# Kernel tuning notes

Hardware: AMD Instinct MI355X
Metric: run time of the kernel (lower is better)

The kernel has to match this reference:

```python
import jax, jax.numpy as jnp
import numpy as np

N = 50000      # nodes per graph batch (per side)
E = 600000     # edges per side
B = 4096       # number of graphs (drug pairs)
D = 128        # node_dim == hidden_dim
K = 128        # kge_dim
R = 86         # rel_total
L = 3          # n_iter
EPS = 1e-5


def setup_inputs() -> dict:
    key = jax.random.key(0)
    ks = jax.random.split(key, 16)
    inp = {}
    inp["x1"] = jax.random.normal(ks[0], (N, D), jnp.float32)
    inp["x2"] = jax.random.normal(ks[1], (N, D), jnp.float32)
    inp["edge_index1"] = jax.random.randint(ks[2], (2, E), 0, N)
    inp["edge_index2"] = jax.random.randint(ks[3], (2, E), 0, N)
    inp["batch1"] = jnp.sort(jax.random.randint(ks[4], (N,), 0, B))
    inp["batch2"] = jnp.sort(jax.random.randint(ks[5], (N,), 0, B))
    inp["rel"] = jax.random.randint(ks[6], (B,), 0, R)
    # SAGEConv params, stacked over L layers (all [D,D] since node_dim==hidden_dim)
    sc = 0.05
    inp["Wl"] = jax.random.normal(ks[7], (L, D, D), jnp.float32) * sc   # lin on aggregated neighbors (has bias)
    inp["bl"] = jnp.zeros((L, D), jnp.float32)
    inp["Wr"] = jax.random.normal(ks[8], (L, D, D), jnp.float32) * sc   # root (self) lin, no bias
    # BatchNorm (eval mode: running stats)
    inp["bn_gamma"] = jnp.ones((L, D), jnp.float32)
    inp["bn_beta"] = jnp.zeros((L, D), jnp.float32)
    inp["bn_mean"] = jnp.zeros((L, D), jnp.float32)
    inp["bn_var"] = jnp.ones((L, D), jnp.float32)
    # relation embedding + final MLP
    inp["kge"] = jax.random.normal(ks[9], (R, K), jnp.float32)
    inp["W1"] = jax.random.normal(ks[10], (2 * D + K, D), jnp.float32) * sc
    inp["b1"] = jnp.zeros((D,), jnp.float32)
    inp["W2"] = jax.random.normal(ks[11], (D, 1), jnp.float32) * sc
    inp["b2"] = jnp.zeros((1,), jnp.float32)
    return inp


def _gnn(x, edge_index, Wl, bl, Wr, g, b, m, v):
    src, dst = edge_index[0], edge_index[1]
    deg = jax.ops.segment_sum(jnp.ones((E,), x.dtype), dst, num_segments=N)
    deg = jnp.maximum(deg, 1.0)[:, None]
    for i in range(L):
        agg = jax.ops.segment_sum(x[src], dst, num_segments=N) / deg  # mean aggregation
        h = agg @ Wl[i] + bl[i] + x @ Wr[i]                           # SAGEConv
        h = (h - m[i]) * (g[i] / jnp.sqrt(v[i] + EPS)) + b[i]         # BN (eval)
        x = jax.nn.relu(h)                                            # dropout = identity (eval)
    return x


def reference(x1, edge_index1, batch1, x2, edge_index2, batch2, rel,
              Wl, bl, Wr, bn_gamma, bn_beta, bn_mean, bn_var,
              kge, W1, b1, W2, b2):
    h1 = _gnn(x1, edge_index1, Wl, bl, Wr, bn_gamma, bn_beta, bn_mean, bn_var)
    h2 = _gnn(x2, edge_index2, Wl, bl, Wr, bn_gamma, bn_beta, bn_mean, bn_var)
    p1 = jax.ops.segment_sum(h1, batch1, num_segments=B)  # global_add_pool
    p2 = jax.ops.segment_sum(h2, batch2, num_segments=B)
    r = kge[rel]                                          # [B, K]
    z = jnp.concatenate([p1, p2, r], axis=-1)             # [B, 2D+K]
    h = jax.nn.relu(z @ W1 + b1)
    out = h @ W2 + b2
    return out.reshape(-1)
```

## Files before the change

kernel.cpp:

```cpp
#include <hip/hip_runtime.h>

#define NN 50000
#define NE 600000
#define NB 4096
#define DD 128
#define EPSV 1e-5f
#define NBKT 196
#define NCHUNK 256
#define CHSZ ((NE + NCHUNK - 1) / NCHUNK)

typedef __bf16 bf16x8 __attribute__((ext_vector_type(8)));
typedef float f32x4 __attribute__((ext_vector_type(4)));

__device__ inline unsigned short f2bf(float f) {
    unsigned u = __float_as_uint(f);
    u = (u + 0x7FFFu + ((u >> 16) & 1u)) >> 16;
    return (unsigned short)u;
}
__device__ inline float bf2f(unsigned short h) {
    return __uint_as_float(((unsigned)h) << 16);
}

__global__ void k_cvt(const float* __restrict__ x1, const float* __restrict__ x2,
                      unsigned short* __restrict__ xh, unsigned short* __restrict__ xl) {
    int i = blockIdx.x * 256 + threadIdx.x;
    if (i >= 2 * NN * 32) return;
    const float* x = (i < NN * 32) ? x1 : x2;
    int j = (i < NN * 32) ? i : i - NN * 32;
    float4 v = ((const float4*)x)[j];
    ushort4 h, l;
    h.x = f2bf(v.x); l.x = f2bf(v.x - bf2f(h.x));
    h.y = f2bf(v.y); l.y = f2bf(v.y - bf2f(h.y));
    h.z = f2bf(v.z); l.z = f2bf(v.z - bf2f(h.z));
    h.w = f2bf(v.w); l.w = f2bf(v.w - bf2f(h.w));
    ((ushort4*)xh)[i] = h;
    ((ushort4*)xl)[i] = l;
}

__global__ void k_wcvt(const float* __restrict__ Wl, const float* __restrict__ Wr,
                       const float* __restrict__ W1, unsigned* __restrict__ wtp) {
    int t = blockIdx.x * 256 + threadIdx.x;
    if (t >= 3 * 128 * 256 + 128 * 384) return;
    float w;
    int idx;
    if (t < 3 * 128 * 256) {
        int k = t & 255;
        int n = (t >> 8) & 127;
        int l = t >> 15;
        w = (k < 128) ? Wl[l * 16384 + k * 128 + n] : Wr[l * 16384 + (k - 128) * 128 + n];
        idx = t;
    } else {
        int u = t - 3 * 128 * 256;
        int n = u / 384;
        int k = u - n * 384;
        w = W1[k * 128 + n];
        idx = t;
    }
    unsigned short h = f2bf(w);
    unsigned short l = f2bf(w - bf2f(h));
    wtp[idx] = ((unsigned)h << 16) | (unsigned)l;
}

__global__ void k_hist(const int* __restrict__ d0, const int* __restrict__ d1,
                       int* __restrict__ bcnt) {
    int side = (blockIdx.x >= NCHUNK) ? 1 : 0;
    int c = blockIdx.x - side * NCHUNK;
    const int* dst = side ? d1 : d0;
    int tid = threadIdx.x;
    __shared__ int h[NBKT];
    for (int i = tid; i < NBKT; i += 256) h[i] = 0;
    __syncthreads();
    int e0 = c * CHSZ, e1 = min(e0 + CHSZ, NE);
    for (int e = e0 + tid; e < e1; e += 256) atomicAdd(&h[dst[e] >> 8], 1);
    __syncthreads();
    int* bc = bcnt + ((size_t)side * NCHUNK + c) * NBKT;
    for (int i = tid; i < NBKT; i += 256) bc[i] = h[i];
}

__global__ void k_s1(int* __restrict__ bcnt, int* __restrict__ btot) {
    int side = (blockIdx.x >= NBKT) ? 1 : 0;
    int b = blockIdx.x - side * NBKT;
    int tid = threadIdx.x;
    int idx = ((size_t)side * NCHUNK + tid) * NBKT + b;
    int v = bcnt[idx];
    int lane = tid & 63, wv = tid >> 6;
    int x = v;
#pragma unroll
    for (int off = 1; off < 64; off <<= 1) {
        int y = __shfl_up(x, off, 64);
        if (lane >= off) x += y;
    }
    __shared__ int ws4[4];
    if (lane == 63) ws4[wv] = x;
    __syncthreads();
    int add = 0;
#pragma unroll
    for (int w = 0; w < 4; w++)
        if (w < wv) add += ws4[w];
    int incl = x + add;
    bcnt[idx] = incl - v;
    if (tid == 255) btot[side * NBKT + b] = incl;
}

__global__ void k_s2(const int* __restrict__ btot, int* __restrict__ bbase,
                     int* __restrict__ ptrC) {
    int side = blockIdx.x;
    int tid = threadIdx.x;
    int v = (tid < NBKT) ? btot[side * NBKT + tid] : 0;
    int lane = tid & 63, wv = tid >> 6;
    int x = v;
#pragma unroll
    for (int off = 1; off < 64; off <<= 1) {
        int y = __shfl_up(x, off, 64);
        if (lane >= off) x += y;
    }
    __shared__ int ws4[4];
    if (lane == 63) ws4[wv] = x;
    __syncthreads();
    int add = 0;
#pragma unroll
    for (int w = 0; w < 4; w++)
        if (w < wv) add += ws4[w];
    int incl = x + add;
    if (tid < NBKT) bbase[side * NBKT + tid] = incl - v;
    if (tid == 0 && side == 1) ptrC[2 * NN] = 2 * NE;
}

__global__ void k_part(const int* __restrict__ s0, const int* __restrict__ d0,
                       const int* __restrict__ s1, const int* __restrict__ d1,
                       const int* __restrict__ bcnt, const int* __restrict__ bbase,
                       int* __restrict__ part) {
    int side = (blockIdx.x >= NCHUNK) ? 1 : 0;
    int c = blockIdx.x - side * NCHUNK;
    const int* src = side ? s1 : s0;
    const int* dst = side ? d1 : d0;
    int tid = threadIdx.x;
    __shared__ int off[NBKT];
    const int* bc = bcnt + ((size_t)side * NCHUNK + c) * NBKT;
    for (int i = tid; i < NBKT; i += 256) off[i] = bbase[side * NBKT + i] + bc[i];
    __syncthreads();
    int e0 = c * CHSZ, e1 = min(e0 + CHSZ, NE);
    int* P = part + (size_t)side * NE;
    int soff = side * NN;
    for (int e = e0 + tid; e < e1; e += 256) {
        int d = dst[e];
        int pos = atomicAdd(&off[d >> 8], 1);
        P[pos] = ((src[e] + soff) << 8) | (d & 255);
    }
}

__global__ void k_csr(const int* __restrict__ part, const int* __restrict__ bbase,
                      int* __restrict__ ptrC, float* __restrict__ invdC,
                      int* __restrict__ csrC) {
    int side = (blockIdx.x >= NBKT) ? 1 : 0;
    int b = blockIdx.x - side * NBKT;
    int tid = threadIdx.x;
    const int* P = part + (size_t)side * NE;
    int base = bbase[side * NBKT + b];
    int endp = (b == NBKT - 1) ? NE : bbase[side * NBKT + b + 1];
    __shared__ int cnt[256];
    cnt[tid] = 0;
    __syncthreads();
    for (int e = base + tid; e < endp; e += 256) atomicAdd(&cnt[P[e] & 255], 1);
    __syncthreads();
    int v = cnt[tid];
    int lane = tid & 63, wv = tid >> 6;
    int x = v;
#pragma unroll
    for (int off = 1; off < 64; off <<= 1) {
        int y = __shfl_up(x, off, 64);
        if (lane >= off) x += y;
    }
    __shared__ int ws4[4];
    if (lane == 63) ws4[wv] = x;
    __syncthreads();
    int add = 0;
#pragma unroll
    for (int w = 0; w < 4; w++)
        if (w < wv) add += ws4[w];
    int excl = x + add - v;
    int node = (b << 8) + tid;
    if (node < NN) {
        ptrC[side * NN + node] = side * NE + base + excl;
        invdC[side * NN + node] = 1.0f / (float)(v > 1 ? v : 1);
    }
    __syncthreads();
    cnt[tid] = excl;
    __syncthreads();
    for (int e = base + tid; e < endp; e += 256) {
        int p = P[e];
        int pos = atomicAdd(&cnt[p & 255], 1);
        csrC[(size_t)side * NE + base + pos] = p >> 8;
    }
}

__global__ void k_gather(const unsigned short* __restrict__ xh, const int* __restrict__ ptr,
                         const int* __restrict__ csr, const float* __restrict__ invd,
                         unsigned short* __restrict__ aggH) {
    int wid = threadIdx.x >> 6;
    int lane = threadIdx.x & 63;
    int q = lane >> 4;
    int c = lane & 15;
    int n = blockIdx.x * 4 + wid;
    if (n >= 2 * NN) return;
    int beg = ptr[n], end = ptr[n + 1];
    float id = invd[n];
    float a[8];
#pragma unroll
    for (int k = 0; k < 8; k++) a[k] = 0.f;

    for (int base = beg; base < end; base += 64) {
        int cnt = min(end - base, 64);
        int idxv = csr[base + min(lane, cnt - 1)];
        for (int e0 = 0; e0 < cnt; e0 += 8) {
            int eA = e0 + q;
            int eB = e0 + 4 + q;
            int iA = __shfl(idxv, eA, 64);
            int iB = __shfl(idxv, eB, 64);
            float wA = (eA < cnt) ? 1.f : 0.f;
            float wB = (eB < cnt) ? 1.f : 0.f;
            uint4 vA = *(const uint4*)(xh + (((unsigned)iA << 7) + (c << 3)));
            uint4 vB = *(const uint4*)(xh + (((unsigned)iB << 7) + (c << 3)));
            a[0] += wA * __uint_as_float(vA.x << 16);
            a[1] += wA * __uint_as_float(vA.x & 0xffff0000u);
            a[2] += wA * __uint_as_float(vA.y << 16);
            a[3] += wA * __uint_as_float(vA.y & 0xffff0000u);
            a[4] += wA * __uint_as_float(vA.z << 16);
            a[5] += wA * __uint_as_float(vA.z & 0xffff0000u);
            a[6] += wA * __uint_as_float(vA.w << 16);
            a[7] += wA * __uint_as_float(vA.w & 0xffff0000u);
            a[0] += wB * __uint_as_float(vB.x << 16);
            a[1] += wB * __uint_as_float(vB.x & 0xffff0000u);
            a[2] += wB * __uint_as_float(vB.y << 16);
            a[3] += wB * __uint_as_float(vB.y & 0xffff0000u);
            a[4] += wB * __uint_as_float(vB.z << 16);
            a[5] += wB * __uint_as_float(vB.z & 0xffff0000u);
            a[6] += wB * __uint_as_float(vB.w << 16);
            a[7] += wB * __uint_as_float(vB.w & 0xffff0000u);
        }
    }
#pragma unroll
    for (int k = 0; k < 8; k++) {
        a[k] += __shfl_xor(a[k], 16, 64);
        a[k] += __shfl_xor(a[k], 32, 64);
    }
    if (q == 0) {
        unsigned short h0 = f2bf(a[0] * id), h1 = f2bf(a[1] * id);
        unsigned short h2 = f2bf(a[2] * id), h3 = f2bf(a[3] * id);
        unsigned short h4 = f2bf(a[4] * id), h5 = f2bf(a[5] * id);
        unsigned short h6 = f2bf(a[6] * id), h7 = f2bf(a[7] * id);
        uint4 o;
        o.x = (unsigned)h0 | ((unsigned)h1 << 16);
        o.y = (unsigned)h2 | ((unsigned)h3 << 16);
        o.z = (unsigned)h4 | ((unsigned)h5 << 16);
        o.w = (unsigned)h6 | ((unsigned)h7 << 16);
        *(uint4*)(aggH + (size_t)n * DD + c * 8) = o;
    }
}

__launch_bounds__(256)
__global__ void k_gemm(const unsigned short* __restrict__ AH,
                       const unsigned short* __restrict__ XH, const unsigned short* __restrict__ XL,
                       const unsigned* __restrict__ Wtp,
                       const float* __restrict__ bl, const float* __restrict__ g,
                       const float* __restrict__ be, const float* __restrict__ mn,
                       const float* __restrict__ vr,
                       unsigned short* __restrict__ OH, unsigned short* __restrict__ OL,
                       float* __restrict__ Of, int f32out) {
    __shared__ __align__(16) unsigned short sA[2][64 * 40];
    __shared__ __align__(16) unsigned short sW[2][64 * 40];
    int tid = threadIdx.x;
    int gx = blockIdx.x;
    int m0 = (gx >> 1) * 64;
    int n0 = (gx & 1) * 64;
    int lane = tid & 63;
    int w = tid >> 6;
    int fm = lane & 15, q = lane >> 4;
    int wr = (w & 1) * 32;
    int wn = (w >> 1) * 32;

    f32x4 acc[2][2];
#pragma unroll
    for (int i = 0; i < 2; i++)
#pragma unroll
        for (int j = 0; j < 2; j++) acc[i][j] = (f32x4){0.f, 0.f, 0.f, 0.f};

    for (int c = 0; c < 8; c++) {
        int isA = (c < 4);
        const unsigned short* SH = isA ? AH : XH;
        const unsigned short* SL = isA ? (const unsigned short*)0 : XL;
        int k0 = (c & 3) * 32;
        int k0W = c * 32;
        __syncthreads();
#pragma unroll
        for (int i = 0; i < 2; i++) {
            int u = tid + 256 * i;
            int row = u >> 3, seg = u & 7;
            int grow = m0 + row;
            size_t goff = (size_t)grow * DD + k0 + seg * 4;
            ushort4 hv = make_ushort4(0, 0, 0, 0);
            if (grow < 2 * NN) hv = *(const ushort4*)(SH + goff);
            *(ushort4*)&sA[0][row * 40 + seg * 4] = hv;
            if (!isA) {
                ushort4 lv = make_ushort4(0, 0, 0, 0);
                if (grow < 2 * NN) lv = *(const ushort4*)(SL + goff);
                *(ushort4*)&sA[1][row * 40 + seg * 4] = lv;
            }
        }
#pragma unroll
        for (int i = 0; i < 2; i++) {
            int u = tid + 256 * i;
            int row = u >> 3, seg = u & 7;
            uint4 val = *(const uint4*)(Wtp + (size_t)(n0 + row) * 256 + k0W + seg * 4);
            ushort4 hi, lo;
            hi.x = val.x >> 16; hi.y = val.y >> 16; hi.z = val.z >> 16; hi.w = val.w >> 16;
            lo.x = val.x & 0xFFFF; lo.y = val.y & 0xFFFF; lo.z = val.z & 0xFFFF; lo.w = val.w & 0xFFFF;
            *(ushort4*)&sW[0][row * 40 + seg * 4] = hi;
            *(ushort4*)&sW[1][row * 40 + seg * 4] = lo;
        }
        __syncthreads();
        bf16x8 afh[2], afl[2];
#pragma unroll
        for (int mt = 0; mt < 2; mt++) {
            int r = wr + mt * 16 + fm;
            afh[mt] = *(const bf16x8*)&sA[0][r * 40 + q * 8];
            if (!isA) afl[mt] = *(const bf16x8*)&sA[1][r * 40 + q * 8];
        }
#pragma unroll
        for (int nt = 0; nt < 2; nt++) {
            int nr = wn + nt * 16 + fm;
            bf16x8 wh = *(const bf16x8*)&sW[0][nr * 40 + q * 8];
            bf16x8 wl = *(const bf16x8*)&sW[1][nr * 40 + q * 8];
#pragma unroll
            for (int mt = 0; mt < 2; mt++) {
                acc[mt][nt] = __builtin_amdgcn_mfma_f32_16x16x32_bf16(afh[mt], wh, acc[mt][nt], 0, 0, 0);
                acc[mt][nt] = __builtin_amdgcn_mfma_f32_16x16x32_bf16(afh[mt], wl, acc[mt][nt], 0, 0, 0);
                if (!isA)
                    acc[mt][nt] = __builtin_amdgcn_mfma_f32_16x16x32_bf16(afl[mt], wh, acc[mt][nt], 0, 0, 0);
            }
        }
    }

    float scv[2], shv[2];
#pragma unroll
    for (int nt = 0; nt < 2; nt++) {
        int jj = n0 + wn + nt * 16 + fm;
        float s = g[jj] * rsqrtf(vr[jj] + EPSV);
        scv[nt] = s;
        shv[nt] = (bl[jj] - mn[jj]) * s + be[jj];
    }
#pragma unroll
    for (int mt = 0; mt < 2; mt++) {
#pragma unroll
        for (int r = 0; r < 4; r++) {
            int grow = m0 + wr + mt * 16 + q * 4 + r;
            if (grow < 2 * NN) {
#pragma unroll
                for (int nt = 0; nt < 2; nt++) {
                    int gcol = n0 + wn + nt * 16 + fm;
                    float o = fmaxf(acc[mt][nt][r] * scv[nt] + shv[nt], 0.f);
                    if (f32out) {
                        Of[(size_t)grow * DD + gcol] = o;
                    } else {
                        unsigned short h = f2bf(o);
                        OH[(size_t)grow * DD + gcol] = h;
                        OL[(size_t)grow * DD + gcol] = f2bf(o - bf2f(h));
                    }
                }
            }
        }
    }
}

__launch_bounds__(128)
__global__ void k_pool2(const float* __restrict__ cf, const int* __restrict__ bt1,
                        const int* __restrict__ bt2, float* __restrict__ ppool) {
    int side = (blockIdx.x >= NB) ? 1 : 0;
    int b = blockIdx.x - side * NB;
    const int* batch = side ? bt2 : bt1;
    const float* h = cf + (size_t)side * NN * DD;
    __shared__ int sr[2];
    if (threadIdx.x < 2) {
        int target = b + (int)threadIdx.x;
        int lo = 0, hi = NN;
        while (lo < hi) {
            int mid = (lo + hi) >> 1;
            if (batch[mid] < target) lo = mid + 1; else hi = mid;
        }
        sr[threadIdx.x] = lo;
    }
    __syncthreads();
    int beg = sr[0], end = sr[1];
    int t = threadIdx.x;
    float acc = 0.f;
    for (int r = beg; r < end; r++) acc += h[(size_t)r * DD + t];
    ppool[((size_t)side * NB + b) * DD + t] = acc;
}

__global__ void k_zb(const float* __restrict__ ppool, const int* __restrict__ rel,
                     const float* __restrict__ kge,
                     unsigned short* __restrict__ zh, unsigned short* __restrict__ zl) {
    int t = blockIdx.x * 256 + threadIdx.x;
    if (t >= NB * 384) return;
    int b = t / 384;
    int j = t - b * 384;
    float v;
    if (j < 128) v = ppool[(size_t)b * DD + j];
    else if (j < 256) v = ppool[(size_t)NB * DD + (size_t)b * DD + (j - 128)];
    else v = kge[(size_t)rel[b] * 128 + (j - 256)];
    unsigned short h = f2bf(v);
    zh[t] = h;
    zl[t] = f2bf(v - bf2f(h));
}

__launch_bounds__(256)
__global__ void k_mlp2(const unsigned short* __restrict__ zh, const unsigned short* __restrict__ zl,
                       const unsigned* __restrict__ w1p,
                       const float* __restrict__ b1, const float* __restrict__ W2,
                       const float* __restrict__ b2, float* __restrict__ out) {
    __shared__ __align__(16) unsigned short sZ[2][32 * 40];
    __shared__ __align__(16) unsigned short sW[2][128 * 40];
    __shared__ float hpart[32][4];
    int tid = threadIdx.x;
    int m0 = blockIdx.x * 32;
    int lane = tid & 63, w = tid >> 6;
    int fm = lane & 15, q = lane >> 4;
    int wn = w * 32;

    f32x4 acc[2][2];
#pragma unroll
    for (int i = 0; i < 2; i++)
#pragma unroll
        for (int j = 0; j < 2; j++) acc[i][j] = (f32x4){0.f, 0.f, 0.f, 0.f};

    for (int c = 0; c < 12; c++) {
        int k0 = c * 32;
        __syncthreads();
        {
            int row = tid >> 3, seg = tid & 7;
            size_t off = (size_t)(m0 + row) * 384 + k0 + seg * 4;
            *(ushort4*)&sZ[0][row * 40 + seg * 4] = *(const ushort4*)(zh + off);
            *(ushort4*)&sZ[1][row * 40 + seg * 4] = *(const ushort4*)(zl + off);
        }
#pragma unroll
        for (int i = 0; i < 4; i++) {
            int u = tid + 256 * i;
            int row = u >> 3, seg = u & 7;
            uint4 val = *(const uint4*)(w1p + (size_t)row * 384 + k0 + seg * 4);
            ushort4 hi, lo;
            hi.x = val.x >> 16; hi.y = val.y >> 16; hi.z = val.z >> 16; hi.w = val.w >> 16;
            lo.x = val.x & 0xFFFF; lo.y = val.y & 0xFFFF; lo.z = val.z & 0xFFFF; lo.w = val.w & 0xFFFF;
            *(ushort4*)&sW[0][row * 40 + seg * 4] = hi;
            *(ushort4*)&sW[1][row * 40 + seg * 4] = lo;
        }
        __syncthreads();
        bf16x8 zfh[2], zfl[2];
#pragma unroll
        for (int mt = 0; mt < 2; mt++) {
            int r = mt * 16 + fm;
            zfh[mt] = *(const bf16x8*)&sZ[0][r * 40 + q * 8];
            zfl[mt] = *(const bf16x8*)&sZ[1][r * 40 + q * 8];
        }
#pragma unroll
        for (int nt = 0; nt < 2; nt++) {
            int nr = wn + nt * 16 + fm;
            bf16x8 wh = *(const bf16x8*)&sW[0][nr * 40 + q * 8];
            bf16x8 wl = *(const bf16x8*)&sW[1][nr * 40 + q * 8];
#pragma unroll
            for (int mt = 0; mt < 2; mt++) {
                acc[mt][nt] = __builtin_amdgcn_mfma_f32_16x16x32_bf16(zfh[mt], wh, acc[mt][nt], 0, 0, 0);
                acc[mt][nt] = __builtin_amdgcn_mfma_f32_16x16x32_bf16(zfh[mt], wl, acc[mt][nt], 0, 0, 0);
                acc[mt][nt] = __builtin_amdgcn_mfma_f32_16x16x32_bf16(zfl[mt], wh, acc[mt][nt], 0, 0, 0);
            }
        }
    }

    float b1v[2], w2v[2];
#pragma unroll
    for (int nt = 0; nt < 2; nt++) {
        int col = wn + nt * 16 + fm;
        b1v[nt] = b1[col];
        w2v[nt] = W2[col];
    }
#pragma unroll
    for (int mt = 0; mt < 2; mt++) {
#pragma unroll
        for (int r = 0; r < 4; r++) {
            float val = 0.f;
#pragma unroll
            for (int nt = 0; nt < 2; nt++)
                val += fmaxf(acc[mt][nt][r] + b1v[nt], 0.f) * w2v[nt];
#pragma unroll
            for (int m = 1; m < 16; m <<= 1) val += __shfl_xor(val, m, 64);
            if (fm == 0) hpart[mt * 16 + q * 4 + r][w] = val;
        }
    }
    __syncthreads();
    if (tid < 32)
        out[m0 + tid] = hpart[tid][0] + hpart[tid][1] + hpart[tid][2] + hpart[tid][3] + b2[0];
}

extern "C" void kernel_launch(void* const* d_in, const int* in_sizes, int n_in,
                              void* d_out, int out_size, void* d_ws, size_t ws_size,
                              hipStream_t stream) {
    const float* x1  = (const float*)d_in[0];
    const float* x2  = (const float*)d_in[1];
    const int*   ei1 = (const int*)d_in[2];
    const int*   ei2 = (const int*)d_in[3];
    const int*   bt1 = (const int*)d_in[4];
    const int*   bt2 = (const int*)d_in[5];
    const int*   rel = (const int*)d_in[6];
    const float* Wl  = (const float*)d_in[7];
    const float* bl  = (const float*)d_in[8];
    const float* Wr  = (const float*)d_in[9];
    const float* g   = (const float*)d_in[10];
    const float* be  = (const float*)d_in[11];
    const float* mn  = (const float*)d_in[12];
    const float* vr  = (const float*)d_in[13];
    const float* kge = (const float*)d_in[14];
    const float* W1  = (const float*)d_in[15];
    const float* b1v = (const float*)d_in[16];
    const float* W2  = (const float*)d_in[17];
    const float* b2v = (const float*)d_in[18];

    char* ws = (char*)d_ws;
    size_t off = 0;
    auto alloc = [&](size_t bytes) {
        void* p = ws + off;
        off += (bytes + 255) & ~(size_t)255;
        return p;
    };
    const size_t PL = (size_t)2 * NN * DD;
    unsigned short* xbufH = (unsigned short*)alloc(PL * 2);
    unsigned short* xbufL = (unsigned short*)alloc(PL * 2);
    unsigned short* obufH = (unsigned short*)alloc(PL * 2);
    unsigned short* obufL = (unsigned short*)alloc(PL * 2);
    unsigned short* aggH  = (unsigned short*)alloc(PL * 2);
    unsigned* wtp  = (unsigned*)alloc((size_t)(3 * 128 * 256 + 128 * 384) * 4);
    float* ppool   = (float*)alloc((size_t)2 * NB * DD * 4);
    unsigned short* zh = (unsigned short*)alloc((size_t)NB * 384 * 2);
    unsigned short* zl = (unsigned short*)alloc((size_t)NB * 384 * 2);
    int*   bcnt    = (int*)alloc((size_t)2 * NCHUNK * NBKT * 4);
    int*   btot    = (int*)alloc((size_t)2 * NBKT * 4);
    int*   bbase   = (int*)alloc((size_t)2 * NBKT * 4);
    int*   part    = (int*)alloc((size_t)2 * NE * 4);
    int*   ptrC    = (int*)alloc((size_t)(2 * NN + 1) * 4);
    float* invdC   = (float*)alloc((size_t)2 * NN * 4);
    int*   csrC    = (int*)alloc((size_t)2 * NE * 4);
    if (off > ws_size) return;

    float* cf = (float*)obufH;

    const int nbCvt   = 12500;
    const int nbNode4 = (2 * NN + 3) / 4;
    const int nbGemm  = ((2 * NN + 63) / 64) * 2;
    const int nbW     = (3 * 128 * 256 + 128 * 384 + 255) / 256;

    k_wcvt<<<nbW, 256, 0, stream>>>(Wl, Wr, W1, wtp);

    k_hist<<<2 * NCHUNK, 256, 0, stream>>>(ei1 + NE, ei2 + NE, bcnt);
    k_s1<<<2 * NBKT, 256, 0, stream>>>(bcnt, btot);
    k_s2<<<2, 256, 0, stream>>>(btot, bbase, ptrC);
    k_part<<<2 * NCHUNK, 256, 0, stream>>>(ei1, ei1 + NE, ei2, ei2 + NE, bcnt, bbase, part);
    k_csr<<<2 * NBKT, 256, 0, stream>>>(part, bbase, ptrC, invdC, csrC);

    k_cvt<<<nbCvt, 256, 0, stream>>>(x1, x2, xbufH, xbufL);

    k_gather<<<nbNode4, 256, 0, stream>>>(xbufH, ptrC, csrC, invdC, aggH);
    k_gemm<<<nbGemm, 256, 0, stream>>>(aggH, xbufH, xbufL, wtp, bl, g, be, mn, vr,
                                       obufH, obufL, (float*)nullptr, 0);
    k_gather<<<nbNode4, 256, 0, stream>>>(obufH, ptrC, csrC, invdC, aggH);
    k_gemm<<<nbGemm, 256, 0, stream>>>(aggH, obufH, obufL, wtp + 32768, bl + 128, g + 128,
                                       be + 128, mn + 128, vr + 128,
                                       xbufH, xbufL, (float*)nullptr, 0);
    k_gather<<<nbNode4, 256, 0, stream>>>(xbufH, ptrC, csrC, invdC, aggH);
    k_gemm<<<nbGemm, 256, 0, stream>>>(aggH, xbufH, xbufL, wtp + 65536, bl + 256, g + 256,
                                       be + 256, mn + 256, vr + 256,
                                       (unsigned short*)nullptr, (unsigned short*)nullptr, cf, 1);

    k_pool2<<<2 * NB, 128, 0, stream>>>(cf, bt1, bt2, ppool);
    k_zb<<<(NB * 384 + 255) / 256, 256, 0, stream>>>(ppool, rel, kge, zh, zl);
    k_mlp2<<<NB / 32, 256, 0, stream>>>(zh, zl, wtp + 98304, b1v, W2, b2v, (float*)d_out);
}
```

Before: 454.5 us.

## Widen GEMM tile to full 128 columns, pre-split weights, fuse pool with z build

The SAGE GEMM now uses one block per 128 rows covering all 128 output columns (4x4 MFMA tiles per wave). Each activation row is loaded once instead of twice, with 16-byte loads in place of 8-byte ones. Weights are pre-laid out as separate hi/lo bf16 planes per K-chunk, so the GEMM copies them straight into shared memory without unpacking. Pooling is fused with building the concatenated bf16 z input, and the gather accumulates into float2 vectors. The larger tile raises register and LDS use per block and halves the block count, which may reduce occupancy.

```diff
diff --git a/kernel.cpp b/kernel.cpp
--- a/kernel.cpp
+++ b/kernel.cpp
@@ -11,6 +11,7 @@
 
 typedef __bf16 bf16x8 __attribute__((ext_vector_type(8)));
 typedef float f32x4 __attribute__((ext_vector_type(4)));
+typedef float f32x2 __attribute__((ext_vector_type(2)));
 
 __device__ inline unsigned short f2bf(float f) {
     unsigned u = __float_as_uint(f);
@@ -38,27 +39,29 @@
 }
 
 __global__ void k_wcvt(const float* __restrict__ Wl, const float* __restrict__ Wr,
-                       const float* __restrict__ W1, unsigned* __restrict__ wtp) {
+                       const float* __restrict__ W1,
+                       unsigned short* __restrict__ wfp, unsigned* __restrict__ w1p) {
     int t = blockIdx.x * 256 + threadIdx.x;
-    if (t >= 3 * 128 * 256 + 128 * 384) return;
-    float w;
-    int idx;
     if (t < 3 * 128 * 256) {
         int k = t & 255;
         int n = (t >> 8) & 127;
         int l = t >> 15;
-        w = (k < 128) ? Wl[l * 16384 + k * 128 + n] : Wr[l * 16384 + (k - 128) * 128 + n];
-        idx = t;
-    } else {
+        float w = (k < 128) ? Wl[l * 16384 + k * 128 + n] : Wr[l * 16384 + (k - 128) * 128 + n];
+        unsigned short h = f2bf(w);
+        unsigned short lo = f2bf(w - bf2f(h));
+        int c = k >> 5, kk = k & 31;
+        size_t base = (size_t)l * 65536 + (size_t)c * 8192 + n * 32 + kk;
+        wfp[base] = h;
+        wfp[base + 4096] = lo;
+    } else if (t < 3 * 128 * 256 + 128 * 384) {
         int u = t - 3 * 128 * 256;
         int n = u / 384;
         int k = u - n * 384;
-        w = W1[k * 128 + n];
-        idx = t;
-    }
-    unsigned short h = f2bf(w);
-    unsigned short l = f2bf(w - bf2f(h));
-    wtp[idx] = ((unsigned)h << 16) | (unsigned)l;
+        float w = W1[k * 128 + n];
+        unsigned short h = f2bf(w);
+        unsigned short l = f2bf(w - bf2f(h));
+        w1p[u] = ((unsigned)h << 16) | (unsigned)l;
+    }
 }
 
 __global__ void k_hist(const int* __restrict__ d0, const int* __restrict__ d1,
@@ -205,9 +208,9 @@
     if (n >= 2 * NN) return;
     int beg = ptr[n], end = ptr[n + 1];
     float id = invd[n];
-    float a[8];
-#pragma unroll
-    for (int k = 0; k < 8; k++) a[k] = 0.f;
+    f32x2 a2[4];
+#pragma unroll
+    for (int k = 0; k < 4; k++) a2[k] = (f32x2){0.f, 0.f};
 
     for (int base = beg; base < end; base += 64) {
         int cnt = min(end - base, 64);
@@ -217,28 +220,25 @@
             int eB = e0 + 4 + q;
             int iA = __shfl(idxv, eA, 64);
             int iB = __shfl(idxv, eB, 64);
-            float wA = (eA < cnt) ? 1.f : 0.f;
-            float wB = (eB < cnt) ? 1.f : 0.f;
+            f32x2 wA2 = (eA < cnt) ? (f32x2){1.f, 1.f} : (f32x2){0.f, 0.f};
+            f32x2 wB2 = (eB < cnt) ? (f32x2){1.f, 1.f} : (f32x2){0.f, 0.f};
             uint4 vA = *(const uint4*)(xh + (((unsigned)iA << 7) + (c << 3)));
             uint4 vB = *(const uint4*)(xh + (((unsigned)iB << 7) + (c << 3)));
-            a[0] += wA * __uint_as_float(vA.x << 16);
-            a[1] += wA * __uint_as_float(vA.x & 0xffff0000u);
-            a[2] += wA * __uint_as_float(vA.y << 16);
-            a[3] += wA * __uint_as_float(vA.y & 0xffff0000u);
-            a[4] += wA * __uint_as_float(vA.z << 16);
-            a[5] += wA * __uint_as_float(vA.z & 0xffff0000u);
-            a[6] += wA * __uint_as_float(vA.w << 16);
-            a[7] += wA * __uint_as_float(vA.w & 0xffff0000u);
-            a[0] += wB * __uint_as_float(vB.x << 16);
-            a[1] += wB * __uint_as_float(vB.x & 0xffff0000u);
-            a[2] += wB * __uint_as_float(vB.y << 16);
-            a[3] += wB * __uint_as_float(vB.y & 0xffff0000u);
-            a[4] += wB * __uint_as_float(vB.z << 16);
-            a[5] += wB * __uint_as_float(vB.z & 0xffff0000u);
-            a[6] += wB * __uint_as_float(vB.w << 16);
-            a[7] += wB * __uint_as_float(vB.w & 0xffff0000u);
-        }
-    }
+            a2[0] += wA2 * (f32x2){__uint_as_float(vA.x << 16), __uint_as_float(vA.x & 0xffff0000u)};
+            a2[1] += wA2 * (f32x2){__uint_as_float(vA.y << 16), __uint_as_float(vA.y & 0xffff0000u)};
+            a2[2] += wA2 * (f32x2){__uint_as_float(vA.z << 16), __uint_as_float(vA.z & 0xffff0000u)};
+            a2[3] += wA2 * (f32x2){__uint_as_float(vA.w << 16), __uint_as_float(vA.w & 0xffff0000u)};
+            a2[0] += wB2 * (f32x2){__uint_as_float(vB.x << 16), __uint_as_float(vB.x & 0xffff0000u)};
+            a2[1] += wB2 * (f32x2){__uint_as_float(vB.y << 16), __uint_as_float(vB.y & 0xffff0000u)};
+            a2[2] += wB2 * (f32x2){__uint_as_float(vB.z << 16), __uint_as_float(vB.z & 0xffff0000u)};
+            a2[3] += wB2 * (f32x2){__uint_as_float(vB.w << 16), __uint_as_float(vB.w & 0xffff0000u)};
+        }
+    }
+    float a[8];
+    a[0] = a2[0][0]; a[1] = a2[0][1];
+    a[2] = a2[1][0]; a[3] = a2[1][1];
+    a[4] = a2[2][0]; a[5] = a2[2][1];
+    a[6] = a2[3][0]; a[7] = a2[3][1];
 #pragma unroll
     for (int k = 0; k < 8; k++) {
         a[k] += __shfl_xor(a[k], 16, 64);
@@ -259,105 +259,101 @@
 }
 
 __launch_bounds__(256)
-__global__ void k_gemm(const unsigned short* __restrict__ AH,
-                       const unsigned short* __restrict__ XH, const unsigned short* __restrict__ XL,
-                       const unsigned* __restrict__ Wtp,
-                       const float* __restrict__ bl, const float* __restrict__ g,
-                       const float* __restrict__ be, const float* __restrict__ mn,
-                       const float* __restrict__ vr,
-                       unsigned short* __restrict__ OH, unsigned short* __restrict__ OL,
-                       float* __restrict__ Of, int f32out) {
-    __shared__ __align__(16) unsigned short sA[2][64 * 40];
-    __shared__ __align__(16) unsigned short sW[2][64 * 40];
-    int tid = threadIdx.x;
-    int gx = blockIdx.x;
-    int m0 = (gx >> 1) * 64;
-    int n0 = (gx & 1) * 64;
-    int lane = tid & 63;
-    int w = tid >> 6;
-    int fm = lane & 15, q = lane >> 4;
-    int wr = (w & 1) * 32;
-    int wn = (w >> 1) * 32;
-
-    f32x4 acc[2][2];
-#pragma unroll
-    for (int i = 0; i < 2; i++)
-#pragma unroll
-        for (int j = 0; j < 2; j++) acc[i][j] = (f32x4){0.f, 0.f, 0.f, 0.f};
+__global__ void k_gemmL(const unsigned short* __restrict__ AH,
+                        const unsigned short* __restrict__ XH, const unsigned short* __restrict__ XL,
+                        const unsigned short* __restrict__ wfp,
+                        const float* __restrict__ bl, const float* __restrict__ g,
+                        const float* __restrict__ be, const float* __restrict__ mn,
+                        const float* __restrict__ vr,
+                        unsigned short* __restrict__ OH, unsigned short* __restrict__ OL,
+                        float* __restrict__ Of, int f32out) {
+    __shared__ __align__(16) unsigned short sA[2][128 * 40];
+    __shared__ __align__(16) unsigned short sW[2][128 * 40];
+    int tid = threadIdx.x;
+    int lane = tid & 63, w = tid >> 6;
+    int fm = lane & 15, kq = lane >> 4;
+    int m0 = blockIdx.x * 128;
+    int wr = (w & 1) * 64;
+    int wn = (w >> 1) * 64;
+
+    f32x4 acc[4][4];
+#pragma unroll
+    for (int i = 0; i < 4; i++)
+#pragma unroll
+        for (int j = 0; j < 4; j++) acc[i][j] = (f32x4){0.f, 0.f, 0.f, 0.f};
 
     for (int c = 0; c < 8; c++) {
         int isA = (c < 4);
-        const unsigned short* SH = isA ? AH : XH;
-        const unsigned short* SL = isA ? (const unsigned short*)0 : XL;
-        int k0 = (c & 3) * 32;
-        int k0W = c * 32;
+        if (c > 0) __syncthreads();
+#pragma unroll
+        for (int i = 0; i < 2; i++) {
+            int s = tid + 256 * i;
+            int row = s >> 2, seg = s & 3;
+            int grow = m0 + row;
+            size_t goff = (size_t)grow * DD + (c & 3) * 32 + seg * 8;
+            if (isA) {
+                uint4 hv = make_uint4(0, 0, 0, 0);
+                if (grow < 2 * NN) hv = *(const uint4*)(AH + goff);
+                *(uint4*)&sA[0][row * 40 + seg * 8] = hv;
+            } else {
+                uint4 hv = make_uint4(0, 0, 0, 0), lv = make_uint4(0, 0, 0, 0);
+                if (grow < 2 * NN) {
+                    hv = *(const uint4*)(XH + goff);
+                    lv = *(const uint4*)(XL + goff);
+                }
+                *(uint4*)&sA[0][row * 40 + seg * 8] = hv;
+                *(uint4*)&sA[1][row * 40 + seg * 8] = lv;
+            }
+        }
+        const unsigned short* wb = wfp + (size_t)c * 8192;
+#pragma unroll
+        for (int i = 0; i < 2; i++) {
+            int s = tid + 256 * i;
+            int row = s >> 2, seg = s & 3;
+            *(uint4*)&sW[0][row * 40 + seg * 8] = *(const uint4*)(wb + s * 8);
+            *(uint4*)&sW[1][row * 40 + seg * 8] = *(const uint4*)(wb + 4096 + s * 8);
+        }
         __syncthreads();
-#pragma unroll
-        for (int i = 0; i < 2; i++) {
-            int u = tid + 256 * i;
-            int row = u >> 3, seg = u & 7;
-            int grow = m0 + row;
-            size_t goff = (size_t)grow * DD + k0 + seg * 4;
-            ushort4 hv = make_ushort4(0, 0, 0, 0);
-            if (grow < 2 * NN) hv = *(const ushort4*)(SH + goff);
-            *(ushort4*)&sA[0][row * 40 + seg * 4] = hv;
-            if (!isA) {
-                ushort4 lv = make_ushort4(0, 0, 0, 0);
-                if (grow < 2 * NN) lv = *(const ushort4*)(SL + goff);
-                *(ushort4*)&sA[1][row * 40 + seg * 4] = lv;
+
+        bf16x8 ah[4], al[4];
+#pragma unroll
+        for (int mt = 0; mt < 4; mt++) {
+            int r = wr + mt * 16 + fm;
+            ah[mt] = *(const bf16x8*)&sA[0][r * 40 + kq * 8];
+            if (!isA) al[mt] = *(const bf16x8*)&sA[1][r * 40 + kq * 8];
+        }
+#pragma unroll
+        for (int nt = 0; nt < 4; nt++) {
+            int nr = wn + nt * 16 + fm;
+            bf16x8 wh = *(const bf16x8*)&sW[0][nr * 40 + kq * 8];
+            bf16x8 wl = *(const bf16x8*)&sW[1][nr * 40 + kq * 8];
+#pragma unroll
+            for (int mt = 0; mt < 4; mt++) {
+                acc[mt][nt] = __builtin_amdgcn_mfma_f32_16x16x32_bf16(ah[mt], wh, acc[mt][nt], 0, 0, 0);
+                acc[mt][nt] = __builtin_amdgcn_mfma_f32_16x16x32_bf16(ah[mt], wl, acc[mt][nt], 0, 0, 0);
+                if (!isA)
+                    acc[mt][nt] = __builtin_amdgcn_mfma_f32_16x16x32_bf16(al[mt], wh, acc[mt][nt], 0, 0, 0);
             }
         }
-#pragma unroll
-        for (int i = 0; i < 2; i++) {
-            int u = tid + 256 * i;
-            int row = u >> 3, seg = u & 7;
-            uint4 val = *(const uint4*)(Wtp + (size_t)(n0 + row) * 256 + k0W + seg * 4);
-            ushort4 hi, lo;
-            hi.x = val.x >> 16; hi.y = val.y >> 16; hi.z = val.z >> 16; hi.w = val.w >> 16;
-            lo.x = val.x & 0xFFFF; lo.y = val.y & 0xFFFF; lo.z = val.z & 0xFFFF; lo.w = val.w & 0xFFFF;
-            *(ushort4*)&sW[0][row * 40 + seg * 4] = hi;
-            *(ushort4*)&sW[1][row * 40 + seg * 4] = lo;
-        }
-        __syncthreads();
-        bf16x8 afh[2], afl[2];
-#pragma unroll
-        for (int mt = 0; mt < 2; mt++) {
-            int r = wr + mt * 16 + fm;
-            afh[mt] = *(const bf16x8*)&sA[0][r * 40 + q * 8];
-            if (!isA) afl[mt] = *(const bf16x8*)&sA[1][r * 40 + q * 8];
-        }
-#pragma unroll
-        for (int nt = 0; nt < 2; nt++) {
-            int nr = wn + nt * 16 + fm;
-            bf16x8 wh = *(const bf16x8*)&sW[0][nr * 40 + q * 8];
-            bf16x8 wl = *(const bf16x8*)&sW[1][nr * 40 + q * 8];
-#pragma unroll
-            for (int mt = 0; mt < 2; mt++) {
-                acc[mt][nt] = __builtin_amdgcn_mfma_f32_16x16x32_bf16(afh[mt], wh, acc[mt][nt], 0, 0, 0);
-                acc[mt][nt] = __builtin_amdgcn_mfma_f32_16x16x32_bf16(afh[mt], wl, acc[mt][nt], 0, 0, 0);
-                if (!isA)
-                    acc[mt][nt] = __builtin_amdgcn_mfma_f32_16x16x32_bf16(afl[mt], wh, acc[mt][nt], 0, 0, 0);
-            }
-        }
-    }
-
-    float scv[2], shv[2];
-#pragma unroll
-    for (int nt = 0; nt < 2; nt++) {
-        int jj = n0 + wn + nt * 16 + fm;
+    }
+
+    float scv[4], shv[4];
+#pragma unroll
+    for (int nt = 0; nt < 4; nt++) {
+        int jj = wn + nt * 16 + fm;
         float s = g[jj] * rsqrtf(vr[jj] + EPSV);
         scv[nt] = s;
         shv[nt] = (bl[jj] - mn[jj]) * s + be[jj];
     }
 #pragma unroll
-    for (int mt = 0; mt < 2; mt++) {
+    for (int mt = 0; mt < 4; mt++) {
 #pragma unroll
         for (int r = 0; r < 4; r++) {
-            int grow = m0 + wr + mt * 16 + q * 4 + r;
+            int grow = m0 + wr + mt * 16 + kq * 4 + r;
             if (grow < 2 * NN) {
 #pragma unroll
-                for (int nt = 0; nt < 2; nt++) {
-                    int gcol = n0 + wn + nt * 16 + fm;
+                for (int nt = 0; nt < 4; nt++) {
+                    int gcol = wn + nt * 16 + fm;
                     float o = fmaxf(acc[mt][nt][r] * scv[nt] + shv[nt], 0.f);
                     if (f32out) {
                         Of[(size_t)grow * DD + gcol] = o;
@@ -373,8 +369,10 @@
 }
 
 __launch_bounds__(128)
-__global__ void k_pool2(const float* __restrict__ cf, const int* __restrict__ bt1,
-                        const int* __restrict__ bt2, float* __restrict__ ppool) {
+__global__ void k_pool2z(const float* __restrict__ cf, const int* __restrict__ bt1,
+                         const int* __restrict__ bt2, const int* __restrict__ rel,
+                         const float* __restrict__ kge,
+                         unsigned short* __restrict__ zh, unsigned short* __restrict__ zl) {
     int side = (blockIdx.x >= NB) ? 1 : 0;
     int b = blockIdx.x - side * NB;
     const int* batch = side ? bt2 : bt1;
@@ -394,23 +392,17 @@
     int t = threadIdx.x;
     float acc = 0.f;
     for (int r = beg; r < end; r++) acc += h[(size_t)r * DD + t];
-    ppool[((size_t)side * NB + b) * DD + t] = acc;
-}
-
-__global__ void k_zb(const float* __restrict__ ppool, const int* __restrict__ rel,
-                     const float* __restrict__ kge,
-                     unsigned short* __restrict__ zh, unsigned short* __restrict__ zl) {
-    int t = blockIdx.x * 256 + threadIdx.x;
-    if (t >= NB * 384) return;
-    int b = t / 384;
-    int j = t - b * 384;
-    float v;
-    if (j < 128) v = ppool[(size_t)b * DD + j];
-    else if (j < 256) v = ppool[(size_t)NB * DD + (size_t)b * DD + (j - 128)];
-    else v = kge[(size_t)rel[b] * 128 + (j - 256)];
-    unsigned short h = f2bf(v);
-    zh[t] = h;
-    zl[t] = f2bf(v - bf2f(h));
+    size_t zo = (size_t)b * 384 + side * 128 + t;
+    unsigned short hh = f2bf(acc);
+    zh[zo] = hh;
+    zl[zo] = f2bf(acc - bf2f(hh));
+    if (side == 0) {
+        float kv = kge[(size_t)rel[b] * 128 + t];
+        size_t zk = (size_t)b * 384 + 256 + t;
+        unsigned short kh = f2bf(kv);
+        zh[zk] = kh;
+        zl[zk] = f2bf(kv - bf2f(kh));
+    }
 }
 
 __launch_bounds__(256)
@@ -536,8 +528,8 @@
     unsigned short* obufH = (unsigned short*)alloc(PL * 2);
     unsigned short* obufL = (unsigned short*)alloc(PL * 2);
     unsigned short* aggH  = (unsigned short*)alloc(PL * 2);
-    unsigned* wtp  = (unsigned*)alloc((size_t)(3 * 128 * 256 + 128 * 384) * 4);
-    float* ppool   = (float*)alloc((size_t)2 * NB * DD * 4);
+    unsigned short* wfp   = (unsigned short*)alloc((size_t)3 * 65536 * 2);
+    unsigned* w1p  = (unsigned*)alloc((size_t)128 * 384 * 4);
     unsigned short* zh = (unsigned short*)alloc((size_t)NB * 384 * 2);
     unsigned short* zl = (unsigned short*)alloc((size_t)NB * 384 * 2);
     int*   bcnt    = (int*)alloc((size_t)2 * NCHUNK * NBKT * 4);
@@ -553,10 +545,10 @@
 
     const int nbCvt   = 12500;
     const int nbNode4 = (2 * NN + 3) / 4;
-    const int nbGemm  = ((2 * NN + 63) / 64) * 2;
+    const int nbGemmL = (2 * NN + 127) / 128;
     const int nbW     = (3 * 128 * 256 + 128 * 384 + 255) / 256;
 
-    k_wcvt<<<nbW, 256, 0, stream>>>(Wl, Wr, W1, wtp);
+    k_wcvt<<<nbW, 256, 0, stream>>>(Wl, Wr, W1, wfp, w1p);
 
     k_hist<<<2 * NCHUNK, 256, 0, stream>>>(ei1 + NE, ei2 + NE, bcnt);
     k_s1<<<2 * NBKT, 256, 0, stream>>>(bcnt, btot);
@@ -567,18 +559,17 @@
     k_cvt<<<nbCvt, 256, 0, stream>>>(x1, x2, xbufH, xbufL);
 
     k_gather<<<nbNode4, 256, 0, stream>>>(xbufH, ptrC, csrC, invdC, aggH);
-    k_gemm<<<nbGemm, 256, 0, stream>>>(aggH, xbufH, xbufL, wtp, bl, g, be, mn, vr,
-                                       obufH, obufL, (float*)nullptr, 0);
+    k_gemmL<<<nbGemmL, 256, 0, stream>>>(aggH, xbufH, xbufL, wfp, bl, g, be, mn, vr,
+                                         obufH, obufL, (float*)nullptr, 0);
     k_gather<<<nbNode4, 256, 0, stream>>>(obufH, ptrC, csrC, invdC, aggH);
-    k_gemm<<<nbGemm, 256, 0, stream>>>(aggH, obufH, obufL, wtp + 32768, bl + 128, g + 128,
-                                       be + 128, mn + 128, vr + 128,
-                                       xbufH, xbufL, (float*)nullptr, 0);
+    k_gemmL<<<nbGemmL, 256, 0, stream>>>(aggH, obufH, obufL, wfp + 65536, bl + 128, g + 128,
+                                         be + 128, mn + 128, vr + 128,
+                                         xbufH, xbufL, (float*)nullptr, 0);
     k_gather<<<nbNode4, 256, 0, stream>>>(xbufH, ptrC, csrC, invdC, aggH);
-    k_gemm<<<nbGemm, 256, 0, stream>>>(aggH, xbufH, xbufL, wtp + 65536, bl + 256, g + 256,
-                                       be + 256, mn + 256, vr + 256,
-                                       (unsigned short*)nullptr, (unsigned short*)nullptr, cf, 1);
-
-    k_pool2<<<2 * NB, 128, 0, stream>>>(cf, bt1, bt2, ppool);
-    k_zb<<<(NB * 384 + 255) / 256, 256, 0, stream>>>(ppool, rel, kge, zh, zl);
-    k_mlp2<<<NB / 32, 256, 0, stream>>>(zh, zl, wtp + 98304, b1v, W2, b2v, (float*)d_out);
-}
+    k_gemmL<<<nbGemmL, 256, 0, stream>>>(aggH, xbufH, xbufL, wfp + 131072, bl + 256, g + 256,
+                                         be + 256, mn + 256, vr + 256,
+                                         (unsigned short*)nullptr, (unsigned short*)nullptr, cf, 1);
+
+    k_pool2z<<<2 * NB, 128, 0, stream>>>(cf, bt1, bt2, rel, kge, zh, zl);
+    k_mlp2<<<NB / 32, 256, 0, stream>>>(zh, zl, w1p, b1v, W2, b2v, (float*)d_out);
+}
```

Result: faster. 445.1 us (-2.1%).
